# Optimization experiments

Hardware: AMD Instinct MI355X
Metric: run time of the kernel (lower is better)

The kernel has to match this reference:

```python
import jax, jax.numpy as jnp
import numpy as np

NUM_LAYERS = 3

def setup_inputs() -> dict:
    key = jax.random.key(0)
    k1, k2, k3, k4 = jax.random.split(key, 4)
    N, D, E = 100000, 128, 3200000
    x = jax.random.normal(k1, (N, D), dtype=jnp.float32)
    edge_row = jax.random.randint(k2, (E,), 0, N, dtype=jnp.int64 if jax.config.jax_enable_x64 else jnp.int32)
    edge_col = jax.random.randint(k3, (E,), 0, N, dtype=jnp.int64 if jax.config.jax_enable_x64 else jnp.int32)
    # normalized-adjacency-like positive values
    edge_val = jax.random.uniform(k4, (E,), dtype=jnp.float32)
    return {"x": x, "edge_row": edge_row, "edge_col": edge_col, "edge_val": edge_val}

def _spmm(edge_row, edge_col, edge_val, emb, num_nodes):
    # out[r] += val * emb[c]  -- sparse adjacency @ emb
    msgs = edge_val[:, None] * emb[edge_col]          # [E, D] gather + scale
    return jax.ops.segment_sum(msgs, edge_row, num_segments=num_nodes)

def reference(x, edge_row, edge_col, edge_val):
    N = x.shape[0]
    emb = x
    acc = x  # running sum over layer embeddings (layer 0 included)
    for _ in range(NUM_LAYERS):
        emb = _spmm(edge_row, edge_col, edge_val, emb, N)
        acc = acc + emb
    # mean over (num_layers + 1) stacked embeddings, without materializing the stack
    return acc / jnp.float32(NUM_LAYERS + 1)
```

## Files before the change

kernel.cpp:

```cpp
#include <hip/hip_runtime.h>

#define DIMS 128
#define RPB 64
#define CAP 3072
#define NBK_MAX 1600

typedef _Float16 half_t;
typedef _Float16 half2_t __attribute__((ext_vector_type(2)));

__global__ void cvt_kernel(const float* __restrict__ src, half_t* __restrict__ dst, int n2) {
    int i = blockIdx.x * blockDim.x + threadIdx.x;
    if (i >= n2) return;
    float2 v = reinterpret_cast<const float2*>(src)[i];
    half2_t h;
    h.x = (half_t)v.x;
    h.y = (half_t)v.y;
    reinterpret_cast<half2_t*>(&dst[0])[i] = h;
}

__global__ __launch_bounds__(256) void binA_kernel(
    const int* __restrict__ row, const int* __restrict__ col,
    const float* __restrict__ val, int E, int nbk,
    int* __restrict__ fill, int2* __restrict__ staged) {
    __shared__ int cnt[NBK_MAX];
    __shared__ int base[NBK_MAX];
    const int t = threadIdx.x;
    const int tile0 = blockIdx.x * (256 * 32);
    for (int j = t; j < nbk; j += 256) cnt[j] = 0;
    __syncthreads();
    for (int k = 0; k < 32; ++k) {
        int e = tile0 + k * 256 + t;
        if (e < E) atomicAdd(&cnt[row[e] >> 6], 1);
    }
    __syncthreads();
    for (int j = t; j < nbk; j += 256) {
        int c = cnt[j];
        base[j] = c ? atomicAdd(&fill[j], c) : 0;
        cnt[j] = 0;
    }
    __syncthreads();
    for (int k = 0; k < 32; ++k) {
        int e = tile0 + k * 256 + t;
        if (e < E) {
            int r = row[e];
            int b = r >> 6;
            int p = base[b] + atomicAdd(&cnt[b], 1);
            if (p < CAP) {
                int2 pk;
                pk.x = ((r & 63) << 24) | col[e];
                pk.y = __float_as_int(val[e]);
                staged[(size_t)b * CAP + p] = pk;
            }
        }
    }
}

__global__ __launch_bounds__(256) void sort_bucket(
    const int* __restrict__ fill, int2* __restrict__ staged,
    int* __restrict__ rowinfo, int N) {
    __shared__ int2 buf[CAP];
    __shared__ int2 outb[CAP];
    __shared__ int ofs_l[RPB];
    const int b = blockIdx.x;
    const int t = threadIdx.x;
    const int cnt = min(fill[b], CAP);
    int2* gb = staged + (size_t)b * CAP;

    for (int i = t; i < cnt; i += 256) buf[i] = gb[i];
    if (t < RPB) ofs_l[t] = 0;
    __syncthreads();
    for (int i = t; i < cnt; i += 256)
        atomicAdd(&ofs_l[((unsigned)buf[i].x) >> 24], 1);
    __syncthreads();
    if (t < 64) {
        int h = ofs_l[t];
        int v = h;
        for (int d = 1; d < 64; d <<= 1) {
            int u = __shfl_up(v, d, 64);
            if (t >= d) v += u;
        }
        int excl = v - h;
        int r = b * RPB + t;
        if (r < N) rowinfo[r] = (excl << 16) | v;
        ofs_l[t] = excl;
    }
    __syncthreads();
    for (int i = t; i < cnt; i += 256) {
        int2 pk = buf[i];
        int p = atomicAdd(&ofs_l[((unsigned)pk.x) >> 24], 1);
        outb[p] = pk;
    }
    __syncthreads();
    for (int i = t; i < cnt; i += 256) gb[i] = outb[i];
}

template <int MODE>
__global__ __launch_bounds__(256) void spmm_kernel(
    const half_t* __restrict__ emb_in, const int* __restrict__ rowinfo,
    const int2* __restrict__ staged, int N,
    half_t* __restrict__ emb_out, float* __restrict__ acc, const float* __restrict__ x) {
    int r = (blockIdx.x * blockDim.x + threadIdx.x) >> 6;
    int lane = threadIdx.x & 63;
    if (r >= N) return;
    int info = rowinfo[r];
    int start = info >> 16;
    int end = info & 0xFFFF;
    const int2* eb = staged + (size_t)(r >> 6) * CAP;
    const int di = lane * 2;

    float ax0 = 0.f, ay0 = 0.f, ax1 = 0.f, ay1 = 0.f;
    float ax2 = 0.f, ay2 = 0.f, ax3 = 0.f, ay3 = 0.f;
    int e = start;
    for (; e + 3 < end; e += 4) {
        int2 p0 = eb[e], p1 = eb[e + 1], p2 = eb[e + 2], p3 = eb[e + 3];
        int c0 = p0.x & 0xFFFFFF, c1 = p1.x & 0xFFFFFF;
        int c2 = p2.x & 0xFFFFFF, c3 = p3.x & 0xFFFFFF;
        half2_t t0 = *reinterpret_cast<const half2_t*>(&emb_in[(size_t)c0 * DIMS + di]);
        half2_t t1 = *reinterpret_cast<const half2_t*>(&emb_in[(size_t)c1 * DIMS + di]);
        half2_t t2 = *reinterpret_cast<const half2_t*>(&emb_in[(size_t)c2 * DIMS + di]);
        half2_t t3 = *reinterpret_cast<const half2_t*>(&emb_in[(size_t)c3 * DIMS + di]);
        float v0 = __int_as_float(p0.y), v1 = __int_as_float(p1.y);
        float v2 = __int_as_float(p2.y), v3 = __int_as_float(p3.y);
        ax0 += v0 * (float)t0.x; ay0 += v0 * (float)t0.y;
        ax1 += v1 * (float)t1.x; ay1 += v1 * (float)t1.y;
        ax2 += v2 * (float)t2.x; ay2 += v2 * (float)t2.y;
        ax3 += v3 * (float)t3.x; ay3 += v3 * (float)t3.y;
    }
    for (; e < end; ++e) {
        int2 p0 = eb[e];
        int c0 = p0.x & 0xFFFFFF;
        half2_t t0 = *reinterpret_cast<const half2_t*>(&emb_in[(size_t)c0 * DIMS + di]);
        float v0 = __int_as_float(p0.y);
        ax0 += v0 * (float)t0.x; ay0 += v0 * (float)t0.y;
    }
    float ax = (ax0 + ax1) + (ax2 + ax3);
    float ay = (ay0 + ay1) + (ay2 + ay3);

    size_t o = (size_t)r * DIMS + di;
    if (MODE == 0 || MODE == 1) {
        half2_t h;
        h.x = (half_t)ax;
        h.y = (half_t)ay;
        *reinterpret_cast<half2_t*>(&emb_out[o]) = h;
    }
    if (MODE == 0) {
        float2 xv = *reinterpret_cast<const float2*>(&x[o]);
        *reinterpret_cast<float2*>(&acc[o]) = make_float2(xv.x + ax, xv.y + ay);
    } else if (MODE == 1) {
        float2 cv = *reinterpret_cast<float2*>(&acc[o]);
        *reinterpret_cast<float2*>(&acc[o]) = make_float2(cv.x + ax, cv.y + ay);
    } else {
        float2 cv = *reinterpret_cast<float2*>(&acc[o]);
        *reinterpret_cast<float2*>(&acc[o]) =
            make_float2((cv.x + ax) * 0.25f, (cv.y + ay) * 0.25f);
    }
}


extern "C" void kernel_launch(void* const* d_in, const int* in_sizes, int n_in,
                              void* d_out, int out_size, void* d_ws, size_t ws_size,
                              hipStream_t stream) {
    const float* x = (const float*)d_in[0];
    const int* erow = (const int*)d_in[1];
    const int* ecol = (const int*)d_in[2];
    const float* eval = (const float*)d_in[3];
    const int N = in_sizes[0] / DIMS;
    const int E = in_sizes[1];
    float* out = (float*)d_out;
    const int nbk = (N + RPB - 1) / RPB;

    char* ws = (char*)d_ws;
    size_t off = 0;
    auto carve = [&](size_t bytes) {
        void* p = ws + off;
        off = (off + bytes + 255) & ~(size_t)255;
        return p;
    };
    half_t* xh = (half_t*)carve((size_t)N * DIMS * sizeof(half_t));
    half_t* embB1 = (half_t*)carve((size_t)N * DIMS * sizeof(half_t));
    half_t* embB2 = (half_t*)carve((size_t)N * DIMS * sizeof(half_t));
    int2* staged = (int2*)carve((size_t)nbk * CAP * sizeof(int2));
    int* fill = (int*)carve((size_t)nbk * sizeof(int));
    int* rowinfo = (int*)carve((size_t)N * sizeof(int));
    (void)ws_size;

    hipMemsetAsync(fill, 0, (size_t)nbk * sizeof(int), stream);
    const int n2 = N * DIMS / 2;
    cvt_kernel<<<(n2 + 255) / 256, 256, 0, stream>>>(x, xh, n2);
    binA_kernel<<<(E + 8191) / 8192, 256, 0, stream>>>(erow, ecol, eval, E, nbk, fill, staged);
    sort_bucket<<<nbk, 256, 0, stream>>>(fill, staged, rowinfo, N);

    const int spmm_blocks = (N + 3) / 4;
    spmm_kernel<0><<<spmm_blocks, 256, 0, stream>>>(xh, rowinfo, staged, N, embB1, out, x);
    spmm_kernel<1><<<spmm_blocks, 256, 0, stream>>>(embB1, rowinfo, staged, N, embB2, out, x);
    spmm_kernel<2><<<spmm_blocks, 256, 0, stream>>>(embB2, rowinfo, staged, N, embB1, out, x);
}
```

Measured before the change: 612.9 us.

## Sort edges by column within rows, unroll gather by 8, store accumulator in fp16

The bucket sort now uses 512 threads and a 1024-bin key of (row, coarse column), so edges within each row are ordered by column range for better gather locality. The SpMM inner loop is unrolled to 8 independent loads and accumulators to raise memory-level parallelism. The running accumulator is kept as fp16 in workspace instead of fp32 in the output, and buffers are reused, which cuts accumulator read/write traffic. The cost is extra fp16 rounding on the accumulator and in x, which lowers accuracy.

```diff
diff --git a/kernel.cpp b/kernel.cpp
--- a/kernel.cpp
+++ b/kernel.cpp
@@ -4,6 +4,7 @@
 #define RPB 64
 #define CAP 3072
 #define NBK_MAX 1600
+#define NBINS 1024
 
 typedef _Float16 half_t;
 typedef _Float16 half2_t __attribute__((ext_vector_type(2)));
@@ -55,50 +56,76 @@
     }
 }
 
-__global__ __launch_bounds__(256) void sort_bucket(
+__global__ __launch_bounds__(512) void sort_bucket(
     const int* __restrict__ fill, int2* __restrict__ staged,
     int* __restrict__ rowinfo, int N) {
     __shared__ int2 buf[CAP];
     __shared__ int2 outb[CAP];
-    __shared__ int ofs_l[RPB];
+    __shared__ int cur[NBINS];
+    __shared__ int wsum[8];
     const int b = blockIdx.x;
     const int t = threadIdx.x;
+    const int w = t >> 6, lane = t & 63;
     const int cnt = min(fill[b], CAP);
     int2* gb = staged + (size_t)b * CAP;
 
-    for (int i = t; i < cnt; i += 256) buf[i] = gb[i];
-    if (t < RPB) ofs_l[t] = 0;
-    __syncthreads();
-    for (int i = t; i < cnt; i += 256)
-        atomicAdd(&ofs_l[((unsigned)buf[i].x) >> 24], 1);
-    __syncthreads();
-    if (t < 64) {
-        int h = ofs_l[t];
-        int v = h;
-        for (int d = 1; d < 64; d <<= 1) {
-            int u = __shfl_up(v, d, 64);
-            if (t >= d) v += u;
+    cur[2 * t] = 0;
+    cur[2 * t + 1] = 0;
+    for (int i = t; i < cnt; i += 512) buf[i] = gb[i];
+    __syncthreads();
+    for (int i = t; i < cnt; i += 512) {
+        unsigned k = (unsigned)buf[i].x;
+        int key = (int)((k >> 24) << 4) | (int)((k & 0xFFFFFF) >> 13);
+        atomicAdd(&cur[key], 1);
+    }
+    __syncthreads();
+    int h0 = cur[2 * t], h1 = cur[2 * t + 1];
+    int s = h0 + h1;
+    int v = s;
+    for (int d = 1; d < 64; d <<= 1) {
+        int u = __shfl_up(v, d, 64);
+        if (lane >= d) v += u;
+    }
+    if (lane == 63) wsum[w] = v;
+    __syncthreads();
+    if (t < 8) {
+        int ws = wsum[t];
+        int vv = ws;
+        for (int d = 1; d < 8; d <<= 1) {
+            int u = __shfl_up(vv, d, 64);
+            if (t >= d) vv += u;
         }
-        int excl = v - h;
+        wsum[t] = vv - ws;
+    }
+    __syncthreads();
+    int excl = wsum[w] + (v - s);
+    cur[2 * t] = excl;
+    cur[2 * t + 1] = excl + h0;
+    __syncthreads();
+    if (t < RPB) {
+        int start = cur[t * 16];
+        int end = (t == RPB - 1) ? cnt : cur[t * 16 + 16];
         int r = b * RPB + t;
-        if (r < N) rowinfo[r] = (excl << 16) | v;
-        ofs_l[t] = excl;
-    }
-    __syncthreads();
-    for (int i = t; i < cnt; i += 256) {
+        if (r < N) rowinfo[r] = (start << 16) | end;
+    }
+    __syncthreads();
+    for (int i = t; i < cnt; i += 512) {
         int2 pk = buf[i];
-        int p = atomicAdd(&ofs_l[((unsigned)pk.x) >> 24], 1);
+        unsigned k = (unsigned)pk.x;
+        int key = (int)((k >> 24) << 4) | (int)((k & 0xFFFFFF) >> 13);
+        int p = atomicAdd(&cur[key], 1);
         outb[p] = pk;
     }
     __syncthreads();
-    for (int i = t; i < cnt; i += 256) gb[i] = outb[i];
+    for (int i = t; i < cnt; i += 512) gb[i] = outb[i];
 }
 
 template <int MODE>
 __global__ __launch_bounds__(256) void spmm_kernel(
     const half_t* __restrict__ emb_in, const int* __restrict__ rowinfo,
     const int2* __restrict__ staged, int N,
-    half_t* __restrict__ emb_out, float* __restrict__ acc, const float* __restrict__ x) {
+    half_t* __restrict__ emb_out, half_t* __restrict__ acc_h,
+    float* __restrict__ out) {
     int r = (blockIdx.x * blockDim.x + threadIdx.x) >> 6;
     int lane = threadIdx.x & 63;
     if (r >= N) return;
@@ -108,51 +135,60 @@
     const int2* eb = staged + (size_t)(r >> 6) * CAP;
     const int di = lane * 2;
 
-    float ax0 = 0.f, ay0 = 0.f, ax1 = 0.f, ay1 = 0.f;
-    float ax2 = 0.f, ay2 = 0.f, ax3 = 0.f, ay3 = 0.f;
+    float ax[8], ay[8];
+#pragma unroll
+    for (int k = 0; k < 8; ++k) { ax[k] = 0.f; ay[k] = 0.f; }
     int e = start;
-    for (; e + 3 < end; e += 4) {
-        int2 p0 = eb[e], p1 = eb[e + 1], p2 = eb[e + 2], p3 = eb[e + 3];
-        int c0 = p0.x & 0xFFFFFF, c1 = p1.x & 0xFFFFFF;
-        int c2 = p2.x & 0xFFFFFF, c3 = p3.x & 0xFFFFFF;
-        half2_t t0 = *reinterpret_cast<const half2_t*>(&emb_in[(size_t)c0 * DIMS + di]);
-        half2_t t1 = *reinterpret_cast<const half2_t*>(&emb_in[(size_t)c1 * DIMS + di]);
-        half2_t t2 = *reinterpret_cast<const half2_t*>(&emb_in[(size_t)c2 * DIMS + di]);
-        half2_t t3 = *reinterpret_cast<const half2_t*>(&emb_in[(size_t)c3 * DIMS + di]);
-        float v0 = __int_as_float(p0.y), v1 = __int_as_float(p1.y);
-        float v2 = __int_as_float(p2.y), v3 = __int_as_float(p3.y);
-        ax0 += v0 * (float)t0.x; ay0 += v0 * (float)t0.y;
-        ax1 += v1 * (float)t1.x; ay1 += v1 * (float)t1.y;
-        ax2 += v2 * (float)t2.x; ay2 += v2 * (float)t2.y;
-        ax3 += v3 * (float)t3.x; ay3 += v3 * (float)t3.y;
+    for (; e + 7 < end; e += 8) {
+        int2 p[8];
+        half2_t t[8];
+#pragma unroll
+        for (int k = 0; k < 8; ++k) p[k] = eb[e + k];
+#pragma unroll
+        for (int k = 0; k < 8; ++k)
+            t[k] = *reinterpret_cast<const half2_t*>(
+                &emb_in[(size_t)(p[k].x & 0xFFFFFF) * DIMS + di]);
+#pragma unroll
+        for (int k = 0; k < 8; ++k) {
+            float v = __int_as_float(p[k].y);
+            ax[k] += v * (float)t[k].x;
+            ay[k] += v * (float)t[k].y;
+        }
     }
     for (; e < end; ++e) {
         int2 p0 = eb[e];
-        int c0 = p0.x & 0xFFFFFF;
-        half2_t t0 = *reinterpret_cast<const half2_t*>(&emb_in[(size_t)c0 * DIMS + di]);
+        half2_t t0 = *reinterpret_cast<const half2_t*>(
+            &emb_in[(size_t)(p0.x & 0xFFFFFF) * DIMS + di]);
         float v0 = __int_as_float(p0.y);
-        ax0 += v0 * (float)t0.x; ay0 += v0 * (float)t0.y;
-    }
-    float ax = (ax0 + ax1) + (ax2 + ax3);
-    float ay = (ay0 + ay1) + (ay2 + ay3);
+        ax[0] += v0 * (float)t0.x;
+        ay[0] += v0 * (float)t0.y;
+    }
+    float axs = ((ax[0] + ax[1]) + (ax[2] + ax[3])) + ((ax[4] + ax[5]) + (ax[6] + ax[7]));
+    float ays = ((ay[0] + ay[1]) + (ay[2] + ay[3])) + ((ay[4] + ay[5]) + (ay[6] + ay[7]));
 
     size_t o = (size_t)r * DIMS + di;
     if (MODE == 0 || MODE == 1) {
         half2_t h;
-        h.x = (half_t)ax;
-        h.y = (half_t)ay;
+        h.x = (half_t)axs;
+        h.y = (half_t)ays;
         *reinterpret_cast<half2_t*>(&emb_out[o]) = h;
     }
     if (MODE == 0) {
-        float2 xv = *reinterpret_cast<const float2*>(&x[o]);
-        *reinterpret_cast<float2*>(&acc[o]) = make_float2(xv.x + ax, xv.y + ay);
+        half2_t xv = *reinterpret_cast<const half2_t*>(&emb_in[o]);
+        half2_t a;
+        a.x = (half_t)((float)xv.x + axs);
+        a.y = (half_t)((float)xv.y + ays);
+        *reinterpret_cast<half2_t*>(&acc_h[o]) = a;
     } else if (MODE == 1) {
-        float2 cv = *reinterpret_cast<float2*>(&acc[o]);
-        *reinterpret_cast<float2*>(&acc[o]) = make_float2(cv.x + ax, cv.y + ay);
+        half2_t cv = *reinterpret_cast<half2_t*>(&acc_h[o]);
+        half2_t a;
+        a.x = (half_t)((float)cv.x + axs);
+        a.y = (half_t)((float)cv.y + ays);
+        *reinterpret_cast<half2_t*>(&acc_h[o]) = a;
     } else {
-        float2 cv = *reinterpret_cast<float2*>(&acc[o]);
-        *reinterpret_cast<float2*>(&acc[o]) =
-            make_float2((cv.x + ax) * 0.25f, (cv.y + ay) * 0.25f);
+        half2_t cv = *reinterpret_cast<half2_t*>(&acc_h[o]);
+        *reinterpret_cast<float2*>(&out[o]) =
+            make_float2(((float)cv.x + axs) * 0.25f, ((float)cv.y + ays) * 0.25f);
     }
 }
 
@@ -178,7 +214,7 @@
     };
     half_t* xh = (half_t*)carve((size_t)N * DIMS * sizeof(half_t));
     half_t* embB1 = (half_t*)carve((size_t)N * DIMS * sizeof(half_t));
-    half_t* embB2 = (half_t*)carve((size_t)N * DIMS * sizeof(half_t));
+    half_t* acc_h = (half_t*)carve((size_t)N * DIMS * sizeof(half_t));
     int2* staged = (int2*)carve((size_t)nbk * CAP * sizeof(int2));
     int* fill = (int*)carve((size_t)nbk * sizeof(int));
     int* rowinfo = (int*)carve((size_t)N * sizeof(int));
@@ -188,10 +224,10 @@
     const int n2 = N * DIMS / 2;
     cvt_kernel<<<(n2 + 255) / 256, 256, 0, stream>>>(x, xh, n2);
     binA_kernel<<<(E + 8191) / 8192, 256, 0, stream>>>(erow, ecol, eval, E, nbk, fill, staged);
-    sort_bucket<<<nbk, 256, 0, stream>>>(fill, staged, rowinfo, N);
+    sort_bucket<<<nbk, 512, 0, stream>>>(fill, staged, rowinfo, N);
 
     const int spmm_blocks = (N + 3) / 4;
-    spmm_kernel<0><<<spmm_blocks, 256, 0, stream>>>(xh, rowinfo, staged, N, embB1, out, x);
-    spmm_kernel<1><<<spmm_blocks, 256, 0, stream>>>(embB1, rowinfo, staged, N, embB2, out, x);
-    spmm_kernel<2><<<spmm_blocks, 256, 0, stream>>>(embB2, rowinfo, staged, N, embB1, out, x);
-}
+    spmm_kernel<0><<<spmm_blocks, 256, 0, stream>>>(xh, rowinfo, staged, N, embB1, acc_h, out);
+    spmm_kernel<1><<<spmm_blocks, 256, 0, stream>>>(embB1, rowinfo, staged, N, xh, acc_h, out);
+    spmm_kernel<2><<<spmm_blocks, 256, 0, stream>>>(xh, rowinfo, staged, N, embB1, acc_h, out);
+}
```

New measurement: 589.8 us. -3.8%, faster.
